# Kernel tuning notes

Hardware: AMD Instinct MI355X
Metric: run time of the kernel (lower is better)

The kernel has to match this reference:

```python
import jax, jax.numpy as jnp
import numpy as np
from jax import lax

B, S, E, CC, H, NH, K = 8, 2048, 128, 256, 256, 8, 7
HD = H // NH  # head dim = 32


def setup_inputs() -> dict:
    key = jax.random.key(0)
    ks = jax.random.split(key, 16)
    x = jax.random.normal(ks[0], (B, S, E), dtype=jnp.float32)
    lengths = jax.random.randint(ks[1], (B,), S // 2, S + 1)
    mask = (jnp.arange(S)[None, :] < lengths[:, None])  # contiguous prefix padding mask
    sc = 0.02
    return {
        "x": x,
        "mask": mask,
        "conv_w": jax.random.normal(ks[2], (CC, E, K), dtype=jnp.float32) * sc,
        "conv_b": jnp.zeros((CC,), jnp.float32),
        "wq": jax.random.normal(ks[3], (CC, H), dtype=jnp.float32) * sc,
        "bq": jnp.zeros((H,), jnp.float32),
        "wk": jax.random.normal(ks[4], (CC, H), dtype=jnp.float32) * sc,
        "bk": jnp.zeros((H,), jnp.float32),
        "wv": jax.random.normal(ks[5], (CC, H), dtype=jnp.float32) * sc,
        "bv": jnp.zeros((H,), jnp.float32),
        "fc_w": jax.random.normal(ks[6], (H, CC), dtype=jnp.float32) * sc,
        "fc_b": jnp.zeros((CC,), jnp.float32),
        "ln_g": jnp.ones((CC,), jnp.float32),
        "ln_b": jnp.zeros((CC,), jnp.float32),
        "gamma": jnp.float32(0.5),
        "std_param": jnp.float32(0.2),
    }


def _penalty(mask, gamma, std_param):
    # (B, S, S) Gaussian penalty, nonzero only in the valid_len x valid_len block
    valid_len = mask.sum(axis=-1).astype(jnp.float32)  # (B,)
    idx = jnp.arange(S, dtype=jnp.float32)
    valid = (jnp.arange(S)[None, :] < mask.sum(axis=-1)[:, None]).astype(jnp.float32)  # (B,S)
    norm_pos = (idx[None, :] + 1.0) / (valid_len[:, None] + 1.0)  # (B,S)
    std = jnp.clip(std_param, 0.01, 0.5)
    base = jnp.exp(-((norm_pos - 0.5) ** 2) / (2.0 * std * std))
    pvec = base * (jnp.exp(gamma) - 1.0) * valid  # (B,S)
    pen = 0.5 * (pvec[:, :, None] + pvec[:, None, :])
    return pen * valid[:, :, None] * valid[:, None, :]


def reference(x, mask, conv_w, conv_b, wq, bq, wk, bk, wv, bv, fc_w, fc_b, ln_g, ln_b, gamma, std_param):
    # Conv1d frontend: (B,S,E) -> (B,E,S) -> conv -> relu -> (B,S,CC)
    xt = jnp.transpose(x, (0, 2, 1))
    y = lax.conv_general_dilated(xt, conv_w, window_strides=(1,), padding=[(K // 2, K // 2)])
    y = jax.nn.relu(y + conv_b[None, :, None])
    h = jnp.transpose(y, (0, 2, 1))  # (B,S,CC)

    q = (h @ wq + bq).reshape(B, S, NH, HD).transpose(0, 2, 1, 3)
    k = (h @ wk + bk).reshape(B, S, NH, HD).transpose(0, 2, 1, 3)
    v = (h @ wv + bv).reshape(B, S, NH, HD).transpose(0, 2, 1, 3)

    scores = jnp.einsum('bnqd,bnkd->bnqk', q, k) / np.sqrt(HD).astype(np.float32)
    scores = scores - _penalty(mask, gamma, std_param)[:, None, :, :]
    scores = jnp.where(mask[:, None, None, :], scores, jnp.float32(-1e10))
    probs = jax.nn.softmax(scores, axis=-1)
    ctx = jnp.einsum('bnqk,bnkd->bnqd', probs, v)
    ctx = ctx.transpose(0, 2, 1, 3).reshape(B, S, H)
    out = ctx @ fc_w + fc_b

    z = h + out
    mu = z.mean(-1, keepdims=True)
    var = ((z - mu) ** 2).mean(-1, keepdims=True)
    return (z - mu) / jnp.sqrt(var + 1e-5) * ln_g + ln_b
```

## Files before the change

### kernel.cpp

```cpp
#include <hip/hip_runtime.h>
#include <hip/hip_bf16.h>

#define B_ 8
#define S_ 2048
#define E_ 128
#define CC_ 256
#define H_ 256
#define NH_ 8
#define HD_ 32
#define KW_ 7

typedef __attribute__((ext_vector_type(8))) short bf16x8;
typedef __attribute__((ext_vector_type(4))) float f32x4;
typedef __attribute__((ext_vector_type(16))) float f32x16;

#define QSCALE_ (0.17677669529663687f * 1.4426950408889634f)
#define CPEN_   0.7213475204444817f

static __device__ __forceinline__ unsigned short f2bf(float f) {
    __hip_bfloat16 h = __float2bfloat16(f);
    return *(unsigned short*)&h;
}
static __device__ __forceinline__ float bf2f(unsigned short u) {
    __hip_bfloat16 h = *(__hip_bfloat16*)&u;
    return __bfloat162float(h);
}
static __device__ __forceinline__ void perm32swap(unsigned& a, unsigned& b) {
    asm volatile("s_nop 1\n\tv_permlane32_swap_b32 %0, %1" : "+v"(a), "+v"(b));
}

__global__ __launch_bounds__(256) void prep_kernel(
    const float* __restrict__ cw, const float* __restrict__ wq,
    const float* __restrict__ wk, const float* __restrict__ wv,
    const float* __restrict__ fw, const void* __restrict__ mask,
    const float* __restrict__ gamma_p, const float* __restrict__ std_p,
    unsigned short* __restrict__ wre2, unsigned short* __restrict__ wqkv2,
    unsigned short* __restrict__ wf2, float* __restrict__ ctab,
    int* __restrict__ lenv)
{
    __shared__ int cnt[256];
    const int blk = blockIdx.x, tid = threadIdx.x;

    if (blk < 896) {
        int i = blk * 256 + tid;
        int kl = i & 31, cc = (i >> 5) & 255, eb = (i >> 13) & 3, kk = i >> 15;
        wre2[i] = f2bf(cw[cc * (E_ * KW_) + (eb * 32 + kl) * KW_ + kk]);
    } else if (blk < 1664) {
        int i = (blk - 896) * 256 + tid;
        int kl = i & 31, col = (i >> 5) & 255, kb = (i >> 13) & 7, m = i >> 16;
        const float* W = (m == 0) ? wq : (m == 1) ? wk : wv;
        wqkv2[i] = f2bf(W[(kb * 32 + kl) * H_ + col]);
    } else if (blk < 1920) {
        int i = (blk - 1664) * 256 + tid;
        int kl = i & 31, col = (i >> 5) & 255, kb = i >> 13;
        wf2[i] = f2bf(fw[(kb * 32 + kl) * CC_ + col]);
    } else {
        int b = blk - 1920;

        uint32_t w0 = ((const uint32_t*)mask)[0];
        int mode = 0;
        if (w0 == 0x01010101u) mode = 1;
        else if (w0 == 0x3F803F80u) mode = 2;
        else if (w0 == 0x3F800000u) mode = 3;

        int c = 0;
        for (int s = tid; s < S_; s += 256) {
            bool vv;
            size_t i = (size_t)b * S_ + s;
            if (mode == 0)      vv = ((const int*)mask)[i] != 0;
            else if (mode == 1) vv = ((const unsigned char*)mask)[i] != 0;
            else if (mode == 2) vv = (((const unsigned short*)mask)[i] & 0x7FFFu) != 0;
            else                vv = ((const float*)mask)[i] != 0.f;
            c += vv ? 1 : 0;
        }
        cnt[tid] = c;
        __syncthreads();
        for (int off = 128; off > 0; off >>= 1) {
            if (tid < off) cnt[tid] += cnt[tid + off];
            __syncthreads();
        }
        int L = cnt[0];
        if (tid == 0) lenv[b] = L;

        float Lf = (float)L;
        float gamma = gamma_p[0];
        float sd = std_p[0];
        sd = fminf(fmaxf(sd, 0.01f), 0.5f);
        float scale = expf(gamma) - 1.f;
        float inv2s2 = 1.f / (2.f * sd * sd);
        float* row0 = ctab + (size_t)b * 2 * S_;
        float* row1 = row0 + S_;
        for (int s = tid; s < S_; s += 256) {
            float np = (s + 1.f) / (Lf + 1.f);
            float e = np - 0.5f;
            float base = expf(-(e * e) * inv2s2);
            bool vkk = s < L;
            row0[s] = vkk ? 0.f : -1e10f;
            row1[s] = vkk ? (-CPEN_ * base * scale) : -1e10f;
        }
    }
}

__global__ __launch_bounds__(256) void front_kernel(
    const float* __restrict__ x, const unsigned short* __restrict__ wre2,
    const float* __restrict__ cb, const unsigned short* __restrict__ wqkv2,
    const float* __restrict__ bq, const float* __restrict__ bk,
    const float* __restrict__ bv, unsigned short* __restrict__ hb,
    unsigned short* __restrict__ qo, unsigned short* __restrict__ ko,
    unsigned short* __restrict__ vo)
{
    __shared__ __align__(16) char smem[64 * 264 * 2];
    short (*xl)[136] = (short(*)[136])smem;
    short (*Al)[264] = (short(*)[264])smem;

    const int tid = threadIdx.x, wave = tid >> 6, lane = tid & 63;
    const int l15 = lane & 15, l4 = lane >> 4;
    const int s0 = blockIdx.x * 64, b = blockIdx.y;

    for (int idx = tid; idx < 70 * 32; idx += 256) {
        int row = idx >> 5, c4 = idx & 31;
        int pos = s0 - 3 + row;
        float4 v = {0.f, 0.f, 0.f, 0.f};
        if (pos >= 0 && pos < S_)
            v = *(const float4*)(x + ((size_t)b * S_ + pos) * E_ + c4 * 4);
        short* p = &xl[row][c4 * 4];
        p[0] = (short)f2bf(v.x); p[1] = (short)f2bf(v.y);
        p[2] = (short)f2bf(v.z); p[3] = (short)f2bf(v.w);
    }
    __syncthreads();

    f32x4 acc[4][4];
#pragma unroll
    for (int i = 0; i < 4; i++)
#pragma unroll
        for (int j = 0; j < 4; j++) acc[i][j] = (f32x4){0.f, 0.f, 0.f, 0.f};

#pragma unroll 1
    for (int kk = 0; kk < KW_; kk++) {
#pragma unroll
        for (int eb = 0; eb < 4; eb++) {
            const unsigned short* wp =
                wre2 + (((size_t)(kk * 4 + eb) * 256 + wave * 64 + l15) * 32) + l4 * 8;
            bf16x8 af[4], bfr[4];
#pragma unroll
            for (int ct = 0; ct < 4; ct++)
                bfr[ct] = *(const bf16x8*)(wp + ct * 512);
#pragma unroll
            for (int rt = 0; rt < 4; rt++)
                af[rt] = *(const bf16x8*)(&xl[rt * 16 + l15 + kk][eb * 32 + l4 * 8]);
#pragma unroll
            for (int rt = 0; rt < 4; rt++)
#pragma unroll
                for (int ct = 0; ct < 4; ct++)
                    acc[rt][ct] = __builtin_amdgcn_mfma_f32_16x16x32_bf16(
                        af[rt], bfr[ct], acc[rt][ct], 0, 0, 0);
        }
    }
    __syncthreads();

#pragma unroll
    for (int ct = 0; ct < 4; ct++) {
        int col = wave * 64 + ct * 16 + l15;
        float bias = cb[col];
#pragma unroll
        for (int rt = 0; rt < 4; rt++)
#pragma unroll
            for (int r = 0; r < 4; r++) {
                float v0 = acc[rt][ct][r] + bias;
                v0 = v0 > 0.f ? v0 : 0.f;
                Al[rt * 16 + l4 * 4 + r][col] = (short)f2bf(v0);
            }
    }
    __syncthreads();

    for (int idx = tid; idx < 64 * 32; idx += 256) {
        int row = idx >> 5, c8 = idx & 31;
        *(bf16x8*)(hb + ((size_t)b * S_ + s0 + row) * CC_ + c8 * 8) =
            *(const bf16x8*)(&Al[row][c8 * 8]);
    }

#pragma unroll 1
    for (int m = 0; m < 3; m++) {
        f32x4 qacc[4][4];
#pragma unroll
        for (int i = 0; i < 4; i++)
#pragma unroll
            for (int j = 0; j < 4; j++) qacc[i][j] = (f32x4){0.f, 0.f, 0.f, 0.f};

#pragma unroll 1
        for (int kb8 = 0; kb8 < 8; kb8++) {
            const unsigned short* wp =
                wqkv2 + (((size_t)(m * 8 + kb8) * 256 + wave * 64 + l15) * 32) + l4 * 8;
            bf16x8 af[4], bfr[4];
#pragma unroll
            for (int ct = 0; ct < 4; ct++)
                bfr[ct] = *(const bf16x8*)(wp + ct * 512);
#pragma unroll
            for (int rt = 0; rt < 4; rt++)
                af[rt] = *(const bf16x8*)(&Al[rt * 16 + l15][kb8 * 32 + l4 * 8]);
#pragma unroll
            for (int rt = 0; rt < 4; rt++)
#pragma unroll
                for (int ct = 0; ct < 4; ct++)
                    qacc[rt][ct] = __builtin_amdgcn_mfma_f32_16x16x32_bf16(
                        af[rt], bfr[ct], qacc[rt][ct], 0, 0, 0);
        }

        const float* bias_p = (m == 0) ? bq : (m == 1) ? bk : bv;
        unsigned short* O = (m == 0) ? qo : (m == 1) ? ko : vo;
        const float oscale = (m == 0) ? QSCALE_ : 1.f;
#pragma unroll
        for (int ct = 0; ct < 4; ct++) {
            int col = wave * 64 + ct * 16 + l15;
            float bias = bias_p[col];
            int n = col >> 5, d = col & 31;
#pragma unroll
            for (int rt = 0; rt < 4; rt++)
#pragma unroll
                for (int r = 0; r < 4; r++) {
                    int row = s0 + rt * 16 + l4 * 4 + r;
                    O[(((size_t)b * NH_ + n) * S_ + row) * HD_ + d] =
                        f2bf((qacc[rt][ct][r] + bias) * oscale);
                }
        }
    }
}

__global__ __launch_bounds__(256) void attn_mfma_kernel(
    const unsigned short* __restrict__ q, const unsigned short* __restrict__ k,
    const unsigned short* __restrict__ v, const float* __restrict__ ctab,
    const int* __restrict__ lenv, unsigned short* __restrict__ ctxb)
{
    __shared__ short Kt[2][128][40];
    __shared__ short Vt[2][32][136];
    __shared__ __align__(16) float ctC[2][2][128];

    const int tid = threadIdx.x;
    const int wave = tid >> 6, lane = tid & 63;
    const int r31 = lane & 31, hi = lane >> 5;
    const int hi8 = hi * 8, hi4 = hi * 4;

    const int qt = blockIdx.x, n = blockIdx.y, b = blockIdx.z;
    const int qrow = qt * 128 + wave * 32 + r31;
    const int L = lenv[b];
    const int nt = (L + 127) >> 7;

    const size_t head = ((size_t)b * NH_ + n) * S_;
    const unsigned short* qbase = q + head * HD_;
    const unsigned short* kbase = k + head * HD_;
    const unsigned short* vbase = v + head * HD_;
    const float* ct0 = ctab + (size_t)b * 2 * S_;
    const float* ct1 = ct0 + S_;

    bf16x8 qf0 = *(const bf16x8*)(qbase + (size_t)qrow * HD_ + hi8);
    bf16x8 qf1 = *(const bf16x8*)(qbase + (size_t)qrow * HD_ + 16 + hi8);
    const int crow = (qrow < L) ? 1 : 0;

    f32x16 acc;
#pragma unroll
    for (int r = 0; r < 16; r++) acc[r] = 0.f;
    float m_r = 0.f, l_r = 0.f;

    const int krow = tid >> 1, kch = (tid & 1) * 16;
    const int d7x2 = 2 * (r31 & 7);
    const int vc = krow >> 3, vk7 = krow & 7;

    bf16x8 kreg0, kreg1, va, vb;
    float c0r = 0.f, c1r = 0.f;

    kreg0 = *(const bf16x8*)(kbase + (size_t)krow * HD_ + kch);
    kreg1 = *(const bf16x8*)(kbase + (size_t)krow * HD_ + kch + 8);
    va    = *(const bf16x8*)(vbase + (size_t)krow * HD_ + kch);
    vb    = *(const bf16x8*)(vbase + (size_t)krow * HD_ + kch + 8);
    if (tid < 128) { c0r = ct0[tid]; c1r = ct1[tid]; }
    {
        *(bf16x8*)(&Kt[0][krow][kch])     = kreg0;
        *(bf16x8*)(&Kt[0][krow][kch + 8]) = kreg1;
#pragma unroll
        for (int i = 0; i < 8; i++) {
            int d0 = kch + i, d1 = kch + 8 + i;
            Vt[0][d0][((((vc - 2 * (d0 & 7)) & 7) | (vc & 8)) << 3) + vk7] = va[i];
            Vt[0][d1][((((vc - 2 * (d1 & 7)) & 7) | (vc & 8)) << 3) + vk7] = vb[i];
        }
        if (tid < 128) { ctC[0][0][tid] = c0r; ctC[0][1][tid] = c1r; }
    }
    __syncthreads();

#pragma unroll 1
    for (int t = 0; t < nt; t++) {
        const int cur = t & 1;
        const int knext = (t + 1) << 7;
        const bool more = (t + 1 < nt);

        if (more) {
            kreg0 = *(const bf16x8*)(kbase + (size_t)(knext + krow) * HD_ + kch);
            kreg1 = *(const bf16x8*)(kbase + (size_t)(knext + krow) * HD_ + kch + 8);
            va    = *(const bf16x8*)(vbase + (size_t)(knext + krow) * HD_ + kch);
            vb    = *(const bf16x8*)(vbase + (size_t)(knext + krow) * HD_ + kch + 8);
            if (tid < 128) { c0r = ct0[knext + tid]; c1r = ct1[knext + tid]; }
        }

        __builtin_amdgcn_s_setprio(1);
        f32x16 sc[4];
#pragma unroll
        for (int t4 = 0; t4 < 4; t4++) {
            bf16x8 kf0 = *(const bf16x8*)(&Kt[cur][t4 * 32 + r31][hi8]);
            bf16x8 kf1 = *(const bf16x8*)(&Kt[cur][t4 * 32 + r31][16 + hi8]);
            f32x16 c0;
#pragma unroll
            for (int g = 0; g < 4; g++) {
                f32x4 cp = *(const f32x4*)(&ctC[cur][crow][t4 * 32 + g * 8 + hi4]);
#pragma unroll
                for (int j = 0; j < 4; j++) c0[g * 4 + j] = cp[j] - m_r;
            }
            f32x16 s1 = __builtin_amdgcn_mfma_f32_32x32x16_bf16(kf0, qf0, c0, 0, 0, 0);
            sc[t4] = __builtin_amdgcn_mfma_f32_32x32x16_bf16(kf1, qf1, s1, 0, 0, 0);
        }
        __builtin_amdgcn_s_setprio(0);

        float mxa[4];
#pragma unroll
        for (int g = 0; g < 4; g++) mxa[g] = -1e30f;
#pragma unroll
        for (int t4 = 0; t4 < 4; t4++)
#pragma unroll
            for (int g = 0; g < 4; g++)
                mxa[g] = fmaxf(fmaxf(fmaxf(mxa[g], sc[t4][g * 4]),
                                     fmaxf(sc[t4][g * 4 + 1], sc[t4][g * 4 + 2])),
                               sc[t4][g * 4 + 3]);
        float pmx = fmaxf(fmaxf(mxa[0], mxa[1]), fmaxf(mxa[2], mxa[3]));
        pmx = fmaxf(pmx, __shfl_xor(pmx, 32, 64));

        float alpha = 1.f;
        if (!__all(pmx <= 8.f)) {
            float d = fmaxf(pmx, 0.f);
            alpha = exp2f(-d);
            m_r += d;
#pragma unroll
            for (int t4 = 0; t4 < 4; t4++)
#pragma unroll
                for (int r = 0; r < 16; r++) sc[t4][r] -= d;
#pragma unroll
            for (int r = 0; r < 16; r++) acc[r] *= alpha;
        }

        float rsa[4] = {0.f, 0.f, 0.f, 0.f};
        unsigned pk[4][8];
#pragma unroll
        for (int t4 = 0; t4 < 4; t4++) {
            float p[16];
#pragma unroll
            for (int g = 0; g < 4; g++)
#pragma unroll
                for (int j = 0; j < 4; j++) {
                    p[g * 4 + j] = exp2f(sc[t4][g * 4 + j]);
                    rsa[g] += p[g * 4 + j];
                }
            unsigned U00 = (unsigned)f2bf(p[0])  | ((unsigned)f2bf(p[1])  << 16);
            unsigned U01 = (unsigned)f2bf(p[2])  | ((unsigned)f2bf(p[3])  << 16);
            unsigned U10 = (unsigned)f2bf(p[4])  | ((unsigned)f2bf(p[5])  << 16);
            unsigned U11 = (unsigned)f2bf(p[6])  | ((unsigned)f2bf(p[7])  << 16);
            unsigned U20 = (unsigned)f2bf(p[8])  | ((unsigned)f2bf(p[9])  << 16);
            unsigned U21 = (unsigned)f2bf(p[10]) | ((unsigned)f2bf(p[11]) << 16);
            unsigned U30 = (unsigned)f2bf(p[12]) | ((unsigned)f2bf(p[13]) << 16);
            unsigned U31 = (unsigned)f2bf(p[14]) | ((unsigned)f2bf(p[15]) << 16);
            perm32swap(U00, U10);
            perm32swap(U01, U11);
            perm32swap(U20, U30);
            perm32swap(U21, U31);
            pk[t4][0] = U00; pk[t4][1] = U01; pk[t4][2] = U10; pk[t4][3] = U11;
            pk[t4][4] = U20; pk[t4][5] = U21; pk[t4][6] = U30; pk[t4][7] = U31;
        }
        float rs = (rsa[0] + rsa[1]) + (rsa[2] + rsa[3]);
        rs += __shfl_xor(rs, 32, 64);
        l_r = l_r * alpha + rs;

        __builtin_amdgcn_s_setprio(1);
#pragma unroll
        for (int t4 = 0; t4 < 4; t4++) {
            union { unsigned u[4]; bf16x8 v8; } pb0, pb1;
            pb0.u[0] = pk[t4][0]; pb0.u[1] = pk[t4][1];
            pb0.u[2] = pk[t4][2]; pb0.u[3] = pk[t4][3];
            pb1.u[0] = pk[t4][4]; pb1.u[1] = pk[t4][5];
            pb1.u[2] = pk[t4][6]; pb1.u[3] = pk[t4][7];
            int c0i = t4 * 4 + hi, c1i = t4 * 4 + 2 + hi;
            bf16x8 vf0 = *(const bf16x8*)(&Vt[cur][r31][(((c0i - d7x2) & 7) | (c0i & 8)) << 3]);
            bf16x8 vf1 = *(const bf16x8*)(&Vt[cur][r31][(((c1i - d7x2) & 7) | (c1i & 8)) << 3]);
            acc = __builtin_amdgcn_mfma_f32_32x32x16_bf16(vf0, pb0.v8, acc, 0, 0, 0);
            acc = __builtin_amdgcn_mfma_f32_32x32x16_bf16(vf1, pb1.v8, acc, 0, 0, 0);
        }
        __builtin_amdgcn_s_setprio(0);

        if (more) {
            const int nxt = cur ^ 1;
            *(bf16x8*)(&Kt[nxt][krow][kch])     = kreg0;
            *(bf16x8*)(&Kt[nxt][krow][kch + 8]) = kreg1;
#pragma unroll
            for (int i = 0; i < 8; i++) {
                int d0 = kch + i, d1 = kch + 8 + i;
                Vt[nxt][d0][((((vc - 2 * (d0 & 7)) & 7) | (vc & 8)) << 3) + vk7] = va[i];
                Vt[nxt][d1][((((vc - 2 * (d1 & 7)) & 7) | (vc & 8)) << 3) + vk7] = vb[i];
            }
            if (tid < 128) { ctC[nxt][0][tid] = c0r; ctC[nxt][1][tid] = c1r; }
            __syncthreads();
        }
    }

    float inv = 1.f / l_r;
    size_t obase = ((size_t)b * S_ + qrow) * H_ + n * HD_;
#pragma unroll
    for (int g = 0; g < 4; g++)
#pragma unroll
        for (int w = 0; w < 2; w++) {
            unsigned uo = (unsigned)f2bf(acc[g * 4 + w * 2] * inv) |
                          ((unsigned)f2bf(acc[g * 4 + w * 2 + 1] * inv) << 16);
            int d = 8 * g + hi4 + 2 * w;
            *(unsigned*)(ctxb + obase + d) = uo;
        }
}

__global__ __launch_bounds__(256) void fc_ln_mfma_kernel(
    const unsigned short* __restrict__ ctxb, const unsigned short* __restrict__ hb,
    const unsigned short* __restrict__ wf2, const float* __restrict__ fb,
    const float* __restrict__ g, const float* __restrict__ bbias,
    float* __restrict__ out)
{
    const int tid = threadIdx.x, wave = tid >> 6, lane = tid & 63;
    const int l15 = lane & 15, l4 = lane >> 4;
    const int s0 = blockIdx.x * 64, b = blockIdx.y;
    const int arow = s0 + wave * 16 + l15;

    bf16x8 af[8];
#pragma unroll
    for (int kb = 0; kb < 8; kb++)
        af[kb] = *(const bf16x8*)(ctxb + (size_t)((size_t)b * S_ + arow) * H_ + kb * 32 + l4 * 8);

    f32x4 acc[16];
#pragma unroll
    for (int ct = 0; ct < 16; ct++) acc[ct] = (f32x4){0.f, 0.f, 0.f, 0.f};

#pragma unroll 1
    for (int kb = 0; kb < 8; kb++) {
        const unsigned short* wp = wf2 + ((size_t)kb * 256 + l15) * 32 + l4 * 8;
#pragma unroll
        for (int ct = 0; ct < 16; ct++) {
            bf16x8 bfr = *(const bf16x8*)(wp + ct * 512);
            acc[ct] = __builtin_amdgcn_mfma_f32_16x16x32_bf16(af[kb], bfr, acc[ct], 0, 0, 0);
        }
    }

    float fbias[16];
#pragma unroll
    for (int ct = 0; ct < 16; ct++) fbias[ct] = fb[ct * 16 + l15];

#pragma unroll
    for (int r = 0; r < 4; r++) {
        int row = s0 + wave * 16 + l4 * 4 + r;
        size_t ro = ((size_t)b * S_ + row) * CC_;
        float z[16];
        float sum = 0.f;
#pragma unroll
        for (int ct = 0; ct < 16; ct++) {
            float zz = acc[ct][r] + fbias[ct] + bf2f(hb[ro + ct * 16 + l15]);
            z[ct] = zz;
            sum += zz;
        }
#pragma unroll
        for (int off = 1; off < 16; off <<= 1) sum += __shfl_xor(sum, off, 64);
        float mu = sum * (1.f / 256.f);
        float vs = 0.f;
#pragma unroll
        for (int ct = 0; ct < 16; ct++) {
            float d = z[ct] - mu;
            z[ct] = d;
            vs += d * d;
        }
#pragma unroll
        for (int off = 1; off < 16; off <<= 1) vs += __shfl_xor(vs, off, 64);
        float inv = rsqrtf(vs * (1.f / 256.f) + 1e-5f);
#pragma unroll
        for (int ct = 0; ct < 16; ct++) {
            int col = ct * 16 + l15;
            out[ro + col] = z[ct] * inv * g[col] + bbias[col];
        }
    }
}

extern "C" void kernel_launch(void* const* d_in, const int* in_sizes, int n_in,
                              void* d_out, int out_size, void* d_ws, size_t ws_size,
                              hipStream_t stream)
{
    const float* x      = (const float*)d_in[0];
    const void*  mask   = d_in[1];
    const float* conv_w = (const float*)d_in[2];
    const float* conv_b = (const float*)d_in[3];
    const float* wq     = (const float*)d_in[4];
    const float* bq     = (const float*)d_in[5];
    const float* wk     = (const float*)d_in[6];
    const float* bk     = (const float*)d_in[7];
    const float* wv     = (const float*)d_in[8];
    const float* bv     = (const float*)d_in[9];
    const float* fc_w   = (const float*)d_in[10];
    const float* fc_b   = (const float*)d_in[11];
    const float* ln_g   = (const float*)d_in[12];
    const float* ln_b   = (const float*)d_in[13];
    const float* gamma  = (const float*)d_in[14];
    const float* stdp   = (const float*)d_in[15];

    char* ws = (char*)d_ws;
    const size_t MB = 1024 * 1024;
    unsigned short* hb    = (unsigned short*)(ws);
    unsigned short* qb    = (unsigned short*)(ws + 8 * MB);
    unsigned short* kb    = (unsigned short*)(ws + 16 * MB);
    unsigned short* vb    = (unsigned short*)(ws + 24 * MB);
    unsigned short* ctxb  = (unsigned short*)(ws + 32 * MB);
    float*          ctab  = (float*)(ws + 40 * MB);
    int*            lenv  = (int*)(ws + 40 * MB + 256 * 1024);
    unsigned short* wre2  = (unsigned short*)(ws + 41 * MB);
    unsigned short* wqkv2 = (unsigned short*)(ws + 42 * MB);
    unsigned short* wf2   = (unsigned short*)(ws + 43 * MB);

    prep_kernel<<<1928, 256, 0, stream>>>(conv_w, wq, wk, wv, fc_w, mask,
                                          gamma, stdp, wre2, wqkv2, wf2,
                                          ctab, lenv);
    dim3 g2(S_ / 64, B_);
    front_kernel<<<g2, 256, 0, stream>>>(x, wre2, conv_b, wqkv2, bq, bk, bv,
                                         hb, qb, kb, vb);
    dim3 ag(S_ / 128, NH_, B_);
    attn_mfma_kernel<<<ag, 256, 0, stream>>>(qb, kb, vb, ctab, lenv, ctxb);
    fc_ln_mfma_kernel<<<g2, 256, 0, stream>>>(ctxb, hb, wf2, fc_b, ln_g, ln_b,
                                              (float*)d_out);
}
```

Measured before the change: 195.8 us.

## Compute softmax row sums with ones-vector MFMA instead of VALU reductions

Drops the per-element VALU summation and cross-lane shuffle for the softmax denominator. Instead it accumulates the row sum through extra MFMAs that multiply an all-ones operand by the bf16 probability tile. It also adds a fast path that skips subtracting the running max when it is still zero, and moves the max shuffle inside the rare rescale branch. This doubles the MFMA count in the PV stage and uses bf16-rounded probabilities for the denominator, which slightly changes numerics.

```diff
diff --git a/kernel.cpp b/kernel.cpp
--- a/kernel.cpp
+++ b/kernel.cpp
@@ -256,10 +256,14 @@
     bf16x8 qf1 = *(const bf16x8*)(qbase + (size_t)qrow * HD_ + 16 + hi8);
     const int crow = (qrow < L) ? 1 : 0;
 
-    f32x16 acc;
-#pragma unroll
-    for (int r = 0; r < 16; r++) acc[r] = 0.f;
-    float m_r = 0.f, l_r = 0.f;
+    bf16x8 ones;
+#pragma unroll
+    for (int i = 0; i < 8; i++) ones[i] = (short)0x3F80;
+
+    f32x16 acc, acc_l;
+#pragma unroll
+    for (int r = 0; r < 16; r++) { acc[r] = 0.f; acc_l[r] = 0.f; }
+    float m_r = 0.f;
 
     const int krow = tid >> 1, kch = (tid & 1) * 16;
     const int d7x2 = 2 * (r31 & 7);
@@ -302,19 +306,36 @@
 
         __builtin_amdgcn_s_setprio(1);
         f32x16 sc[4];
-#pragma unroll
-        for (int t4 = 0; t4 < 4; t4++) {
-            bf16x8 kf0 = *(const bf16x8*)(&Kt[cur][t4 * 32 + r31][hi8]);
-            bf16x8 kf1 = *(const bf16x8*)(&Kt[cur][t4 * 32 + r31][16 + hi8]);
-            f32x16 c0;
-#pragma unroll
-            for (int g = 0; g < 4; g++) {
-                f32x4 cp = *(const f32x4*)(&ctC[cur][crow][t4 * 32 + g * 8 + hi4]);
-#pragma unroll
-                for (int j = 0; j < 4; j++) c0[g * 4 + j] = cp[j] - m_r;
+        if (__all(m_r == 0.f)) {
+#pragma unroll
+            for (int t4 = 0; t4 < 4; t4++) {
+                bf16x8 kf0 = *(const bf16x8*)(&Kt[cur][t4 * 32 + r31][hi8]);
+                bf16x8 kf1 = *(const bf16x8*)(&Kt[cur][t4 * 32 + r31][16 + hi8]);
+                f32x16 c0;
+#pragma unroll
+                for (int g = 0; g < 4; g++) {
+                    f32x4 cp = *(const f32x4*)(&ctC[cur][crow][t4 * 32 + g * 8 + hi4]);
+#pragma unroll
+                    for (int j = 0; j < 4; j++) c0[g * 4 + j] = cp[j];
+                }
+                f32x16 s1 = __builtin_amdgcn_mfma_f32_32x32x16_bf16(kf0, qf0, c0, 0, 0, 0);
+                sc[t4] = __builtin_amdgcn_mfma_f32_32x32x16_bf16(kf1, qf1, s1, 0, 0, 0);
             }
-            f32x16 s1 = __builtin_amdgcn_mfma_f32_32x32x16_bf16(kf0, qf0, c0, 0, 0, 0);
-            sc[t4] = __builtin_amdgcn_mfma_f32_32x32x16_bf16(kf1, qf1, s1, 0, 0, 0);
+        } else {
+#pragma unroll
+            for (int t4 = 0; t4 < 4; t4++) {
+                bf16x8 kf0 = *(const bf16x8*)(&Kt[cur][t4 * 32 + r31][hi8]);
+                bf16x8 kf1 = *(const bf16x8*)(&Kt[cur][t4 * 32 + r31][16 + hi8]);
+                f32x16 c0;
+#pragma unroll
+                for (int g = 0; g < 4; g++) {
+                    f32x4 cp = *(const f32x4*)(&ctC[cur][crow][t4 * 32 + g * 8 + hi4]);
+#pragma unroll
+                    for (int j = 0; j < 4; j++) c0[g * 4 + j] = cp[j] - m_r;
+                }
+                f32x16 s1 = __builtin_amdgcn_mfma_f32_32x32x16_bf16(kf0, qf0, c0, 0, 0, 0);
+                sc[t4] = __builtin_amdgcn_mfma_f32_32x32x16_bf16(kf1, qf1, s1, 0, 0, 0);
+            }
         }
         __builtin_amdgcn_s_setprio(0);
 
@@ -329,12 +350,11 @@
                                      fmaxf(sc[t4][g * 4 + 1], sc[t4][g * 4 + 2])),
                                sc[t4][g * 4 + 3]);
         float pmx = fmaxf(fmaxf(mxa[0], mxa[1]), fmaxf(mxa[2], mxa[3]));
-        pmx = fmaxf(pmx, __shfl_xor(pmx, 32, 64));
-
-        float alpha = 1.f;
+
         if (!__all(pmx <= 8.f)) {
+            pmx = fmaxf(pmx, __shfl_xor(pmx, 32, 64));
             float d = fmaxf(pmx, 0.f);
-            alpha = exp2f(-d);
+            float alpha = exp2f(-d);
             m_r += d;
 #pragma unroll
             for (int t4 = 0; t4 < 4; t4++)
@@ -342,38 +362,26 @@
                 for (int r = 0; r < 16; r++) sc[t4][r] -= d;
 #pragma unroll
             for (int r = 0; r < 16; r++) acc[r] *= alpha;
-        }
-
-        float rsa[4] = {0.f, 0.f, 0.f, 0.f};
+            acc_l[0] *= alpha;
+        }
+
         unsigned pk[4][8];
 #pragma unroll
         for (int t4 = 0; t4 < 4; t4++) {
-            float p[16];
-#pragma unroll
-            for (int g = 0; g < 4; g++)
-#pragma unroll
-                for (int j = 0; j < 4; j++) {
-                    p[g * 4 + j] = exp2f(sc[t4][g * 4 + j]);
-                    rsa[g] += p[g * 4 + j];
-                }
-            unsigned U00 = (unsigned)f2bf(p[0])  | ((unsigned)f2bf(p[1])  << 16);
-            unsigned U01 = (unsigned)f2bf(p[2])  | ((unsigned)f2bf(p[3])  << 16);
-            unsigned U10 = (unsigned)f2bf(p[4])  | ((unsigned)f2bf(p[5])  << 16);
-            unsigned U11 = (unsigned)f2bf(p[6])  | ((unsigned)f2bf(p[7])  << 16);
-            unsigned U20 = (unsigned)f2bf(p[8])  | ((unsigned)f2bf(p[9])  << 16);
-            unsigned U21 = (unsigned)f2bf(p[10]) | ((unsigned)f2bf(p[11]) << 16);
-            unsigned U30 = (unsigned)f2bf(p[12]) | ((unsigned)f2bf(p[13]) << 16);
-            unsigned U31 = (unsigned)f2bf(p[14]) | ((unsigned)f2bf(p[15]) << 16);
-            perm32swap(U00, U10);
-            perm32swap(U01, U11);
-            perm32swap(U20, U30);
-            perm32swap(U21, U31);
-            pk[t4][0] = U00; pk[t4][1] = U01; pk[t4][2] = U10; pk[t4][3] = U11;
-            pk[t4][4] = U20; pk[t4][5] = U21; pk[t4][6] = U30; pk[t4][7] = U31;
-        }
-        float rs = (rsa[0] + rsa[1]) + (rsa[2] + rsa[3]);
-        rs += __shfl_xor(rs, 32, 64);
-        l_r = l_r * alpha + rs;
+            unsigned U[8];
+#pragma unroll
+            for (int j = 0; j < 8; j++) {
+                float pa = exp2f(sc[t4][2 * j]);
+                float pb = exp2f(sc[t4][2 * j + 1]);
+                U[j] = (unsigned)f2bf(pa) | ((unsigned)f2bf(pb) << 16);
+            }
+            perm32swap(U[0], U[2]);
+            perm32swap(U[1], U[3]);
+            perm32swap(U[4], U[6]);
+            perm32swap(U[5], U[7]);
+            pk[t4][0] = U[0]; pk[t4][1] = U[1]; pk[t4][2] = U[2]; pk[t4][3] = U[3];
+            pk[t4][4] = U[4]; pk[t4][5] = U[5]; pk[t4][6] = U[6]; pk[t4][7] = U[7];
+        }
 
         __builtin_amdgcn_s_setprio(1);
 #pragma unroll
@@ -386,8 +394,10 @@
             int c0i = t4 * 4 + hi, c1i = t4 * 4 + 2 + hi;
             bf16x8 vf0 = *(const bf16x8*)(&Vt[cur][r31][(((c0i - d7x2) & 7) | (c0i & 8)) << 3]);
             bf16x8 vf1 = *(const bf16x8*)(&Vt[cur][r31][(((c1i - d7x2) & 7) | (c1i & 8)) << 3]);
-            acc = __builtin_amdgcn_mfma_f32_32x32x16_bf16(vf0, pb0.v8, acc, 0, 0, 0);
-            acc = __builtin_amdgcn_mfma_f32_32x32x16_bf16(vf1, pb1.v8, acc, 0, 0, 0);
+            acc   = __builtin_amdgcn_mfma_f32_32x32x16_bf16(vf0, pb0.v8, acc, 0, 0, 0);
+            acc_l = __builtin_amdgcn_mfma_f32_32x32x16_bf16(ones, pb0.v8, acc_l, 0, 0, 0);
+            acc   = __builtin_amdgcn_mfma_f32_32x32x16_bf16(vf1, pb1.v8, acc, 0, 0, 0);
+            acc_l = __builtin_amdgcn_mfma_f32_32x32x16_bf16(ones, pb1.v8, acc_l, 0, 0, 0);
         }
         __builtin_amdgcn_s_setprio(0);
 
@@ -406,7 +416,7 @@
         }
     }
 
-    float inv = 1.f / l_r;
+    float inv = 1.f / acc_l[0];
     size_t obase = ((size_t)b * S_ + qrow) * H_ + n * HD_;
 #pragma unroll
     for (int g = 0; g < 4; g++)
```

After: 188.0 us. 4.0% less time.
